# Performance work log

Measured on AMD Instinct MI355X. Metric: run time of the kernel, lower is better.

The kernel has to match this reference:

```python
import jax, jax.numpy as jnp
import numpy as np

K, A, DIM = 1024, 16384, 512


def setup_inputs() -> dict:
    key = jax.random.key(0)
    ks = jax.random.split(key, 8)
    B, H, W = 2048, 8, 8
    z_t = jax.random.randint(ks[0], (B, H, W), 0, K, dtype=jnp.int64)
    z_tp1 = jax.random.randint(ks[1], (B, H, W), 0, K, dtype=jnp.int64)
    embed_w = jax.random.normal(ks[2], (K, DIM), dtype=jnp.float32) * 0.02
    # MLP: Linear(2*dim -> dim), GELU, Linear(dim -> dim)
    lim1 = 1.0 / np.sqrt(2 * DIM)
    w1 = jax.random.uniform(ks[3], (2 * DIM, DIM), minval=-lim1, maxval=lim1, dtype=jnp.float32)
    b1 = jax.random.uniform(ks[4], (DIM,), minval=-lim1, maxval=lim1, dtype=jnp.float32)
    lim2 = 1.0 / np.sqrt(DIM)
    w2 = jax.random.uniform(ks[5], (DIM, DIM), minval=-lim2, maxval=lim2, dtype=jnp.float32)
    b2 = jax.random.uniform(ks[6], (DIM,), minval=-lim2, maxval=lim2, dtype=jnp.float32)
    codebook_w = jax.random.normal(ks[7], (A, DIM), dtype=jnp.float32) * 0.02
    return {"z_t": z_t, "z_tp1": z_tp1, "embed_w": embed_w, "w1": w1, "b1": b1,
            "w2": w2, "b2": b2, "codebook_w": codebook_w}


def reference(z_t, z_tp1, embed_w, w1, b1, w2, b2, codebook_w):
    B = z_t.shape[0]
    # embed int code grids and mean-pool over H*W tokens -> [B, dim]
    e_t = embed_w[z_t.reshape(B, -1)].mean(axis=1)
    e_tp1 = embed_w[z_tp1.reshape(B, -1)].mean(axis=1)
    h = jnp.concatenate([e_t, e_tp1], axis=-1)          # [B, 2*dim]
    h = jax.nn.gelu(h @ w1 + b1, approximate=False)
    e = h @ w2 + b2                                      # [B, dim]
    # VQ: squared L2 distance to each code, argmin, gather
    d2 = (jnp.sum(e * e, axis=1, keepdims=True)
          - 2.0 * e @ codebook_w.T
          + jnp.sum(codebook_w * codebook_w, axis=1)[None, :])  # [B, A]
    ids = jnp.argmin(d2, axis=1)                         # [B]
    q = codebook_w[ids]                                  # [B, dim]
    return ids, q
```

## Files before the change

### kernel.cpp

```cpp
#include <hip/hip_runtime.h>
#include <hip/hip_bf16.h>

#define TOK 64
#define DIMC 512

typedef __attribute__((ext_vector_type(8))) short v8s;
typedef __attribute__((ext_vector_type(4))) float v4f;

#define MFMA16 __builtin_amdgcn_mfma_f32_16x16x32_bf16

__device__ __forceinline__ unsigned int f2ord(float f) {
  unsigned int u = __float_as_uint(f);
  return (u & 0x80000000u) ? ~u : (u | 0x80000000u);
}

__device__ __forceinline__ float gelu_exact(float x) {
  return 0.5f * x * (1.0f + erff(x * 0.70710678118654752440f));
}

__device__ __forceinline__ unsigned short f2bf(float x) {
  unsigned int u = __float_as_uint(x);
  return (unsigned short)((u + 0x7FFFu + ((u >> 16) & 1u)) >> 16);
}
__device__ __forceinline__ float bf2f(unsigned short h) {
  return __uint_as_float((unsigned int)h << 16);
}

__device__ __forceinline__ void gl2lds16(const void* g, void* l) {
  __builtin_amdgcn_global_load_lds((const __attribute__((address_space(1))) void*)g,
                                   (__attribute__((address_space(3))) void*)l,
                                   16, 0, 0);
}

__global__ __launch_bounds__(256) void k_prep(
    const int* __restrict__ zt, const int* __restrict__ ztp,
    const float* __restrict__ emb,
    unsigned short* __restrict__ hh, unsigned short* __restrict__ hl,
    unsigned long long* __restrict__ rowmin,
    const float* __restrict__ w1, unsigned short* __restrict__ w1th,
    unsigned short* __restrict__ w1tl,
    const float* __restrict__ w2, unsigned short* __restrict__ w2th,
    unsigned short* __restrict__ w2tl,
    const float* __restrict__ cb, unsigned short* __restrict__ ch,
    unsigned short* __restrict__ cl, float* __restrict__ cnorm) {
  __shared__ int codes[128];
  __shared__ float tbuf[32][33];
  const int bid = blockIdx.x;
  const int tid = threadIdx.x;

  if (bid < 2048) {
    const int b = bid;
    if (tid < 64) codes[tid] = zt[b * TOK + tid];
    else if (tid < 128) codes[tid] = ztp[b * TOK + (tid - 64)];
    if (tid == 0) rowmin[b] = 0xFFFFFFFFFFFFFFFFull;
    __syncthreads();
    const int half = tid >> 7;
    const int c4 = tid & 127;
    const float4* emb4 = (const float4*)emb;
    float4 s = make_float4(0.f, 0.f, 0.f, 0.f);
    #pragma unroll 8
    for (int t = 0; t < TOK; t++) {
      const int code = codes[half * TOK + t];
      const float4 v = emb4[code * 128 + c4];
      s.x += v.x; s.y += v.y; s.z += v.z; s.w += v.w;
    }
    const float inv = 1.0f / 64.0f;
    float f[4] = {s.x * inv, s.y * inv, s.z * inv, s.w * inv};
    unsigned short hi[4], lo[4];
    #pragma unroll
    for (int i = 0; i < 4; i++) {
      hi[i] = f2bf(f[i]);
      lo[i] = f2bf(f[i] - bf2f(hi[i]));
    }
    const int off = b * 1024 + half * 512 + c4 * 4;
    *(ushort4*)&hh[off] = make_ushort4(hi[0], hi[1], hi[2], hi[3]);
    *(ushort4*)&hl[off] = make_ushort4(lo[0], lo[1], lo[2], lo[3]);
  } else if (bid < 2816) {
    const float* w; unsigned short *wth, *wtl; int Kd, N, k0, n0;
    if (bid < 2560) {
      const int i = bid - 2048;
      w = w1; wth = w1th; wtl = w1tl; Kd = 1024; N = 512;
      k0 = (i & 31) * 32; n0 = (i >> 5) * 32;
    } else {
      const int i = bid - 2560;
      w = w2; wth = w2th; wtl = w2tl; Kd = 512; N = 512;
      k0 = (i & 15) * 32; n0 = (i >> 4) * 32;
    }
    const int c = tid & 31, r = tid >> 5;
    #pragma unroll
    for (int i = 0; i < 4; i++)
      tbuf[r + i * 8][c] = w[(size_t)(k0 + r + i * 8) * N + n0 + c];
    __syncthreads();
    #pragma unroll
    for (int i = 0; i < 4; i++) {
      const float v = tbuf[c][r + i * 8];
      const unsigned short hi = f2bf(v);
      const unsigned short lo = f2bf(v - bf2f(hi));
      wth[(size_t)(n0 + r + i * 8) * Kd + k0 + c] = hi;
      wtl[(size_t)(n0 + r + i * 8) * Kd + k0 + c] = lo;
    }
  } else {
    const int row = (bid - 2816) * 4 + (tid >> 6);
    const int lane = tid & 63;
    const float4* cb4 = (const float4*)cb;
    const float4 va = cb4[row * 128 + lane * 2];
    const float4 vb = cb4[row * 128 + lane * 2 + 1];
    float s = va.x * va.x + va.y * va.y + va.z * va.z + va.w * va.w
            + vb.x * vb.x + vb.y * vb.y + vb.z * vb.z + vb.w * vb.w;
    float f[8] = {va.x, va.y, va.z, va.w, vb.x, vb.y, vb.z, vb.w};
    unsigned short hi[8], lo[8];
    #pragma unroll
    for (int i = 0; i < 8; i++) {
      hi[i] = f2bf(f[i]);
      lo[i] = f2bf(f[i] - bf2f(hi[i]));
    }
    ushort4* chp = (ushort4*)&ch[row * DIMC + lane * 8];
    ushort4* clp = (ushort4*)&cl[row * DIMC + lane * 8];
    chp[0] = make_ushort4(hi[0], hi[1], hi[2], hi[3]);
    chp[1] = make_ushort4(hi[4], hi[5], hi[6], hi[7]);
    clp[0] = make_ushort4(lo[0], lo[1], lo[2], lo[3]);
    clp[1] = make_ushort4(lo[4], lo[5], lo[6], lo[7]);
    #pragma unroll
    for (int off = 32; off > 0; off >>= 1) s += __shfl_down(s, off);
    if (lane == 0) cnorm[row] = s;
  }
}

template <bool GELU>
__global__ __launch_bounds__(256) void k_gemm(const unsigned short* __restrict__ Ah_,
                                              const unsigned short* __restrict__ Al_,
                                              const unsigned short* __restrict__ Bh_,
                                              const unsigned short* __restrict__ Bl_,
                                              const float* __restrict__ bias,
                                              unsigned short* __restrict__ oh,
                                              unsigned short* __restrict__ ol,
                                              int Kd, int N) {
  __shared__ unsigned short AhS[2][32 * 32];
  __shared__ unsigned short AlS[2][32 * 32];
  __shared__ unsigned short BhS[2][64 * 32];
  __shared__ unsigned short BlS[2][64 * 32];

  const int tid = threadIdx.x;
  const int lane = tid & 63;
  const int wid = tid >> 6;
  const int m0 = blockIdx.x * 32;
  const int n0 = blockIdx.y * 64;

  const unsigned short* Ab_h = Ah_ + (size_t)m0 * Kd;
  const unsigned short* Ab_l = Al_ + (size_t)m0 * Kd;
  const unsigned short* Bb_h = Bh_ + (size_t)n0 * Kd;
  const unsigned short* Bb_l = Bl_ + (size_t)n0 * Kd;

  const int srow = lane >> 2;
  const int sk = (lane & 3) * 8;
  const int wm = wid >> 1, wn = wid & 1;
  const int fr = lane & 15;
  const int fq = (lane >> 4) * 8;

  v4f acc[2];
  acc[0] = (v4f)(0.f);
  acc[1] = (v4f)(0.f);

  auto stage = [&](int b, int k0) {
    #pragma unroll
    for (int u = 0; u < 3; u++) {
      const int i = wid * 3 + u;
      const unsigned short* gs; unsigned short* ls; int rbase;
      if (i < 2)      { gs = Ab_h; ls = AhS[b]; rbase = i * 16; }
      else if (i < 4) { gs = Ab_l; ls = AlS[b]; rbase = (i - 2) * 16; }
      else if (i < 8) { gs = Bb_h; ls = BhS[b]; rbase = (i - 4) * 16; }
      else            { gs = Bb_l; ls = BlS[b]; rbase = (i - 8) * 16; }
      gl2lds16(gs + (size_t)(rbase + srow) * Kd + k0 + sk, ls + rbase * 32);
    }
  };

  stage(0, 0);
  int cur = 0;
  for (int k0 = 0; k0 < Kd; k0 += 32) {
    __syncthreads();
    if (k0 + 32 < Kd) stage(cur ^ 1, k0 + 32);

    const int ar = (wm * 16 + fr) * 32 + fq;
    const v8s ah = *(const v8s*)&AhS[cur][ar];
    const v8s al = *(const v8s*)&AlS[cur][ar];
    #pragma unroll
    for (int nt = 0; nt < 2; nt++) {
      const int br = (wn * 32 + nt * 16 + fr) * 32 + fq;
      const v8s bh = *(const v8s*)&BhS[cur][br];
      const v8s bl = *(const v8s*)&BlS[cur][br];
      acc[nt] = MFMA16(ah, bh, acc[nt], 0, 0, 0);
      acc[nt] = MFMA16(ah, bl, acc[nt], 0, 0, 0);
      acc[nt] = MFMA16(al, bh, acc[nt], 0, 0, 0);
    }
    cur ^= 1;
  }

  const int col16 = lane & 15;
  const int q = lane >> 4;
  #pragma unroll
  for (int nt = 0; nt < 2; nt++) {
    const int col = n0 + wn * 32 + nt * 16 + col16;
    const float bv = bias[col];
    #pragma unroll
    for (int reg = 0; reg < 4; reg++) {
      const int row = m0 + wm * 16 + q * 4 + reg;
      float v = acc[nt][reg] + bv;
      if (GELU) v = gelu_exact(v);
      const unsigned short hi = f2bf(v);
      oh[(size_t)row * N + col] = hi;
      ol[(size_t)row * N + col] = f2bf(v - bf2f(hi));
    }
  }
}

__global__ __launch_bounds__(512, 2) void k_vq(const unsigned short* __restrict__ eh,
                                               const unsigned short* __restrict__ el,
                                               const unsigned short* __restrict__ ch,
                                               const unsigned short* __restrict__ cl,
                                               const float* __restrict__ cnorm,
                                               unsigned long long* __restrict__ rowmin) {
  __shared__ unsigned short lds[2 * 32768];

  const int tid = threadIdx.x;
  const int lane = tid & 63;
  const int wid = tid >> 6;
  const int bid = blockIdx.x;
  const int x = (bid >> 3) & 7;
  const int y = (((bid >> 6) & 7) << 3) | (bid & 7);
  const int r0 = x * 256;
  const int c0 = y * 256;

  const unsigned short* ehB = eh + (size_t)r0 * DIMC;
  const unsigned short* elB = el + (size_t)r0 * DIMC;
  const unsigned short* chB = ch + (size_t)c0 * DIMC;
  const unsigned short* clB = cl + (size_t)c0 * DIMC;

  const int srow = lane >> 2;
  const int sk = ((lane & 3) ^ ((lane >> 3) & 3)) * 8;
  const int wm = wid >> 1;
  const int wn = wid & 1;
  const int fr = lane & 15;
  const int q = lane >> 4;
  const int fqs = (q ^ ((fr >> 1) & 3)) * 8;

  v4f acc[4][8];
  #pragma unroll
  for (int i = 0; i < 4; i++)
    #pragma unroll
    for (int jj = 0; jj < 8; jj++) acc[i][jj] = (v4f)(0.f);

  const unsigned short* gp[8];
  int lo_[8];
  #pragma unroll
  for (int u = 0; u < 8; u++) {
    const int i = wid * 8 + u;
    const unsigned short* gs; int off, rbase;
    if (i < 16)      { gs = ehB; off = 0;     rbase = i * 16; }
    else if (i < 32) { gs = elB; off = 8192;  rbase = (i - 16) * 16; }
    else if (i < 48) { gs = chB; off = 16384; rbase = (i - 32) * 16; }
    else             { gs = clB; off = 24576; rbase = (i - 48) * 16; }
    gp[u] = gs + (size_t)(rbase + srow) * DIMC + sk;
    lo_[u] = off + rbase * 32;
  }

  auto stage = [&](int buf, int k0) {
    #pragma unroll
    for (int u = 0; u < 8; u++)
      gl2lds16(gp[u] + k0, lds + buf * 32768 + lo_[u]);
  };

  stage(0, 0);
  __syncthreads();

  for (int t = 0; t < 16; ++t) {
    if (t < 15) stage((t + 1) & 1, (t + 1) * 32);

    const unsigned short* base = lds + (t & 1) * 32768;
    v8s ah[4], al[4];
    #pragma unroll
    for (int mt = 0; mt < 4; mt++) {
      const int ar = (wm * 64 + mt * 16 + fr) * 32 + fqs;
      ah[mt] = *(const v8s*)&base[ar];
      al[mt] = *(const v8s*)&base[8192 + ar];
    }
    __builtin_amdgcn_s_setprio(1);
    #pragma unroll
    for (int nt = 0; nt < 8; nt++) {
      const int br = (wn * 128 + nt * 16 + fr) * 32 + fqs;
      const v8s bh = *(const v8s*)&base[16384 + br];
      const v8s bl = *(const v8s*)&base[24576 + br];
      #pragma unroll
      for (int mt = 0; mt < 4; mt++) {
        acc[mt][nt] = MFMA16(ah[mt], bh, acc[mt][nt], 0, 0, 0);
        acc[mt][nt] = MFMA16(ah[mt], bl, acc[mt][nt], 0, 0, 0);
        acc[mt][nt] = MFMA16(al[mt], bh, acc[mt][nt], 0, 0, 0);
      }
    }
    __builtin_amdgcn_s_setprio(0);
    if (t < 15) __syncthreads();
  }

  const int col16 = lane & 15;
  float cn[8];
  #pragma unroll
  for (int nt = 0; nt < 8; nt++) cn[nt] = cnorm[c0 + wn * 128 + nt * 16 + col16];

  #pragma unroll
  for (int mt = 0; mt < 4; mt++) {
    #pragma unroll
    for (int reg = 0; reg < 4; reg++) {
      const int row = r0 + wm * 64 + mt * 16 + q * 4 + reg;
      float best = fmaf(-2.f, acc[mt][0][reg], cn[0]);
      int bid2 = c0 + wn * 128 + col16;
      #pragma unroll
      for (int nt = 1; nt < 8; nt++) {
        const float s = fmaf(-2.f, acc[mt][nt][reg], cn[nt]);
        const int id = c0 + wn * 128 + nt * 16 + col16;
        if (s < best) { best = s; bid2 = id; }
      }
      unsigned long long v =
          ((unsigned long long)f2ord(best) << 32) | (unsigned int)bid2;
      #pragma unroll
      for (int off = 8; off > 0; off >>= 1) {
        const unsigned long long o = __shfl_down(v, off, 16);
        if (o < v) v = o;
      }
      if (col16 == 0) atomicMin(&rowmin[row], v);
    }
  }
}

__global__ __launch_bounds__(64) void k_final(const unsigned long long* __restrict__ rowmin,
                                              const float* __restrict__ cb,
                                              float* __restrict__ out,
                                              int B) {
  const int b = blockIdx.x;
  const int t = threadIdx.x;
  const unsigned long long m = rowmin[b];
  const int id = (int)(unsigned int)(m & 0xFFFFFFFFull);
  if (t == 0) out[b] = (float)id;
  float4* q4 = (float4*)(out + B) + b * 128;
  const float4* cb4 = (const float4*)cb + (size_t)id * 128;
  q4[t] = cb4[t];
  q4[t + 64] = cb4[t + 64];
}

extern "C" void kernel_launch(void* const* d_in, const int* in_sizes, int n_in,
                              void* d_out, int out_size, void* d_ws, size_t ws_size,
                              hipStream_t stream) {
  const int* zt = (const int*)d_in[0];
  const int* ztp = (const int*)d_in[1];
  const float* emb = (const float*)d_in[2];
  const float* w1 = (const float*)d_in[3];
  const float* b1 = (const float*)d_in[4];
  const float* w2 = (const float*)d_in[5];
  const float* b2 = (const float*)d_in[6];
  const float* cb = (const float*)d_in[7];
  float* out = (float*)d_out;

  const int B = in_sizes[0] / TOK;
  const int A = in_sizes[7] / DIMC;

  char* p = (char*)d_ws;
  unsigned short* hh = (unsigned short*)p;  p += (size_t)B * 1024 * 2;
  unsigned short* hl = (unsigned short*)p;  p += (size_t)B * 1024 * 2;
  unsigned short* w1th = (unsigned short*)p; p += (size_t)512 * 1024 * 2;
  unsigned short* w1tl = (unsigned short*)p; p += (size_t)512 * 1024 * 2;
  unsigned short* w2th = (unsigned short*)p; p += (size_t)512 * 512 * 2;
  unsigned short* w2tl = (unsigned short*)p; p += (size_t)512 * 512 * 2;
  unsigned short* h1h = (unsigned short*)p; p += (size_t)B * DIMC * 2;
  unsigned short* h1l = (unsigned short*)p; p += (size_t)B * DIMC * 2;
  unsigned short* eh = (unsigned short*)p;  p += (size_t)B * DIMC * 2;
  unsigned short* el = (unsigned short*)p;  p += (size_t)B * DIMC * 2;
  unsigned short* ch = (unsigned short*)p;  p += (size_t)A * DIMC * 2;
  unsigned short* cl = (unsigned short*)p;  p += (size_t)A * DIMC * 2;
  float* cnorm = (float*)p;                 p += (size_t)A * 4;
  unsigned long long* rowmin = (unsigned long long*)p;

  k_prep<<<2816 + A / 4, 256, 0, stream>>>(zt, ztp, emb, hh, hl, rowmin,
                                           w1, w1th, w1tl, w2, w2th, w2tl,
                                           cb, ch, cl, cnorm);
  k_gemm<true><<<dim3(B / 32, 512 / 64), 256, 0, stream>>>(hh, hl, w1th, w1tl, b1, h1h, h1l, 1024, 512);
  k_gemm<false><<<dim3(B / 32, 512 / 64), 256, 0, stream>>>(h1h, h1l, w2th, w2tl, b2, eh, el, 512, 512);
  k_vq<<<(B / 256) * (A / 256), 512, 0, stream>>>(eh, el, ch, cl, cnorm, rowmin);
  k_final<<<B, 64, 0, stream>>>(rowmin, cb, out, B);
}
```

Measured before the change: 220.5 us.

## Double K-step per barrier and XOR-swizzle LDS layout in MLP GEMM

```diff
diff --git a/kernel.cpp b/kernel.cpp
--- a/kernel.cpp
+++ b/kernel.cpp
@@ -135,10 +135,10 @@
                                               unsigned short* __restrict__ oh,
                                               unsigned short* __restrict__ ol,
                                               int Kd, int N) {
-  __shared__ unsigned short AhS[2][32 * 32];
-  __shared__ unsigned short AlS[2][32 * 32];
-  __shared__ unsigned short BhS[2][64 * 32];
-  __shared__ unsigned short BlS[2][64 * 32];
+  __shared__ unsigned short AhS[2][2048];
+  __shared__ unsigned short AlS[2][2048];
+  __shared__ unsigned short BhS[2][4096];
+  __shared__ unsigned short BlS[2][4096];
 
   const int tid = threadIdx.x;
   const int lane = tid & 63;
@@ -152,10 +152,11 @@
   const unsigned short* Bb_l = Bl_ + (size_t)n0 * Kd;
 
   const int srow = lane >> 2;
-  const int sk = (lane & 3) * 8;
+  const int sk = ((lane & 3) ^ ((lane >> 3) & 3)) * 8;
   const int wm = wid >> 1, wn = wid & 1;
   const int fr = lane & 15;
-  const int fq = (lane >> 4) * 8;
+  const int q = lane >> 4;
+  const int fqs = (q ^ ((fr >> 1) & 3)) * 8;
 
   v4f acc[2];
   acc[0] = (v4f)(0.f);
@@ -163,40 +164,43 @@
 
   auto stage = [&](int b, int k0) {
     #pragma unroll
-    for (int u = 0; u < 3; u++) {
-      const int i = wid * 3 + u;
-      const unsigned short* gs; unsigned short* ls; int rbase;
-      if (i < 2)      { gs = Ab_h; ls = AhS[b]; rbase = i * 16; }
-      else if (i < 4) { gs = Ab_l; ls = AlS[b]; rbase = (i - 2) * 16; }
-      else if (i < 8) { gs = Bb_h; ls = BhS[b]; rbase = (i - 4) * 16; }
-      else            { gs = Bb_l; ls = BlS[b]; rbase = (i - 8) * 16; }
-      gl2lds16(gs + (size_t)(rbase + srow) * Kd + k0 + sk, ls + rbase * 32);
+    for (int u = 0; u < 6; u++) {
+      const int i = wid * 6 + u;
+      const unsigned short* gs; unsigned short* ls; int slab, seg, rstride;
+      if (i < 4)       { gs = Ab_h; ls = AhS[b]; slab = i >> 1;         seg = i & 1;         rstride = 1024; }
+      else if (i < 8)  { gs = Ab_l; ls = AlS[b]; slab = (i - 4) >> 1;   seg = (i - 4) & 1;   rstride = 1024; }
+      else if (i < 16) { gs = Bb_h; ls = BhS[b]; slab = (i - 8) >> 2;   seg = (i - 8) & 3;   rstride = 2048; }
+      else             { gs = Bb_l; ls = BlS[b]; slab = (i - 16) >> 2;  seg = (i - 16) & 3;  rstride = 2048; }
+      gl2lds16(gs + (size_t)(seg * 16 + srow) * Kd + k0 + slab * 32 + sk,
+               ls + slab * rstride + seg * 512);
     }
   };
 
   stage(0, 0);
   int cur = 0;
-  for (int k0 = 0; k0 < Kd; k0 += 32) {
+  for (int k0 = 0; k0 < Kd; k0 += 64) {
     __syncthreads();
-    if (k0 + 32 < Kd) stage(cur ^ 1, k0 + 32);
-
-    const int ar = (wm * 16 + fr) * 32 + fq;
-    const v8s ah = *(const v8s*)&AhS[cur][ar];
-    const v8s al = *(const v8s*)&AlS[cur][ar];
-    #pragma unroll
-    for (int nt = 0; nt < 2; nt++) {
-      const int br = (wn * 32 + nt * 16 + fr) * 32 + fq;
-      const v8s bh = *(const v8s*)&BhS[cur][br];
-      const v8s bl = *(const v8s*)&BlS[cur][br];
-      acc[nt] = MFMA16(ah, bh, acc[nt], 0, 0, 0);
-      acc[nt] = MFMA16(ah, bl, acc[nt], 0, 0, 0);
-      acc[nt] = MFMA16(al, bh, acc[nt], 0, 0, 0);
+    if (k0 + 64 < Kd) stage(cur ^ 1, k0 + 64);
+
+    #pragma unroll
+    for (int kk = 0; kk < 2; kk++) {
+      const int ar = kk * 1024 + (wm * 16 + fr) * 32 + fqs;
+      const v8s ah = *(const v8s*)&AhS[cur][ar];
+      const v8s al = *(const v8s*)&AlS[cur][ar];
+      #pragma unroll
+      for (int nt = 0; nt < 2; nt++) {
+        const int br = kk * 2048 + (wn * 32 + nt * 16 + fr) * 32 + fqs;
+        const v8s bh = *(const v8s*)&BhS[cur][br];
+        const v8s bl = *(const v8s*)&BlS[cur][br];
+        acc[nt] = MFMA16(ah, bh, acc[nt], 0, 0, 0);
+        acc[nt] = MFMA16(ah, bl, acc[nt], 0, 0, 0);
+        acc[nt] = MFMA16(al, bh, acc[nt], 0, 0, 0);
+      }
     }
     cur ^= 1;
   }
 
   const int col16 = lane & 15;
-  const int q = lane >> 4;
   #pragma unroll
   for (int nt = 0; nt < 2; nt++) {
     const int col = n0 + wn * 32 + nt * 16 + col16;
```

Result: no change. 222.0 us (+0.7%).
